# Performance work log

Measured on AMD Instinct MI355X. Metric: run time of the kernel, lower is better.

## Reference

```python
import jax, jax.numpy as jnp
import numpy as np

N = 8192
LATENT_DIM = 64


def setup_inputs() -> dict:
    key = jax.random.key(0)
    kx, ky = jax.random.split(key)
    x = jax.random.normal(kx, (N, LATENT_DIM), dtype=jnp.float32)
    y = jax.random.normal(ky, (N, LATENT_DIM), dtype=jnp.float32)
    return {"x": x, "y": y}


def _rbf_kernel(a, b):
    # Faithful to torch: exp(-mean((a_i - b_j)^2, axis=dim) / dim)
    #                  = exp(-||a_i - b_j||^2 / dim^2)
    # Computed via the expanded-sq-dist identity to avoid the [N, N, dim]
    # tiled intermediate the torch code materializes.
    dim = a.shape[1]
    sq_a = jnp.sum(a * a, axis=1)  # [Na]
    sq_b = jnp.sum(b * b, axis=1)  # [Nb]
    sq_dist = sq_a[:, None] + sq_b[None, :] - 2.0 * (a @ b.T)  # [Na, Nb]
    return jnp.exp(-sq_dist / (dim * dim))


def reference(x, y):
    # MMD with RBF kernel: mean k(x,x) + mean k(y,y) - 2 mean k(x,y)
    kxx = jnp.mean(_rbf_kernel(x, x))
    kyy = jnp.mean(_rbf_kernel(y, y))
    kxy = jnp.mean(_rbf_kernel(x, y))
    return kxx + kyy - 2.0 * kxy
```

## Files before the change

### kernel.cpp

```cpp
#include <hip/hip_runtime.h>
#include <cmath>

#define NPTS 8192
#define DIM 64
#define BT 128
#define KSTR 132

#define LEAF_F   0
#define LEAF_N   (3 * 8192 * 64)
#define ROWS_F   (LEAF_F + LEAF_N)
#define ROWS_N   (3 * 8192)
#define MEANS_F  (ROWS_F + ROWS_N)
#define NX_F     ((MEANS_F + 3 + 3) & ~3)
#define NY_F     (NX_F + 8192)
#define SPLIT_F  (NY_F + 8192)
#define SPLIT_ELEMS (NPTS * DIM)


typedef short bf16x8 __attribute__((ext_vector_type(8)));
typedef float f32x4  __attribute__((ext_vector_type(4)));
typedef float f32x2  __attribute__((ext_vector_type(2)));

__device__ __forceinline__ unsigned short f32_bf16_rne(float f) {
    unsigned u = __float_as_uint(f);
    return (unsigned short)((u + 0x7FFFu + ((u >> 16) & 1u)) >> 16);
}
__device__ __forceinline__ float bf16_f32(unsigned short h) {
    return __uint_as_float(((unsigned)h) << 16);
}

__global__ void prep_kernel(const float* __restrict__ x, const float* __restrict__ y,
                            unsigned short* __restrict__ Xh, unsigned short* __restrict__ Xl,
                            unsigned short* __restrict__ Yh, unsigned short* __restrict__ Yl,
                            float* __restrict__ nx, float* __restrict__ ny) {
    int r = blockIdx.x * 256 + threadIdx.x;
    int isY = r >= NPTS;
    int rr = isY ? r - NPTS : r;
    const float4* Rg = (const float4*)((isY ? y : x) + (size_t)rr * DIM);
    unsigned short* Hh = isY ? Yh : Xh;
    unsigned short* Hl = isY ? Yl : Xl;
    const int t16 = rr >> 4, mrow = rr & 15;
    float s = 0.f;
    #pragma unroll
    for (int k4 = 0; k4 < 16; ++k4) {
        float4 v = Rg[k4];
        ushort4 h, l;
        h.x = f32_bf16_rne(v.x); l.x = f32_bf16_rne(v.x - bf16_f32(h.x));
        h.y = f32_bf16_rne(v.y); l.y = f32_bf16_rne(v.y - bf16_f32(h.y));
        h.z = f32_bf16_rne(v.z); l.z = f32_bf16_rne(v.z - bf16_f32(h.z));
        h.w = f32_bf16_rne(v.w); l.w = f32_bf16_rne(v.w - bf16_f32(h.w));
        int off = t16 * 1024 + (k4 >> 3) * 512 + ((k4 >> 1) & 3) * 128 + mrow * 8 + (k4 & 1) * 4;
        *(ushort4*)(Hh + off) = h;
        *(ushort4*)(Hl + off) = l;
        s = fmaf(v.x, v.x, s); s = fmaf(v.y, v.y, s);
        s = fmaf(v.z, v.z, s); s = fmaf(v.w, v.w, s);
    }
    if (isY) ny[rr] = s; else nx[rr] = s;
}

__global__ __launch_bounds__(512, 4) void mmd_tile_kernel(
    const unsigned short* __restrict__ Xh, const unsigned short* __restrict__ Xl,
    const unsigned short* __restrict__ Yh, const unsigned short* __restrict__ Yl,
    const float* __restrict__ nx, const float* __restrict__ ny,
    float* __restrict__ leafs)
{
    const int gi = blockIdx.x;
    const int gj = blockIdx.y;
    int zz, bx, by;
    if (blockIdx.z == 1) {
        if (gi >= 64) return;
        zz = 2; bx = gi; by = gj;
    } else if (gi > gj) {
        zz = 0; by = gj; bx = gi - 1;
    } else {
        zz = 1; by = gi; bx = gj;
    }

    __shared__ __align__(16) float Ks[128 * KSTR];
    __shared__ float sqA[BT];
    __shared__ float sqB[BT];

    const int t = threadIdx.x;
    const size_t arow = (size_t)by * BT;
    const size_t brow = (size_t)bx * BT;
    const int cb = bx;

    const unsigned short* pAh = (zz == 1) ? Yh : Xh;
    const unsigned short* pAl = (zz == 1) ? Yl : Xl;
    const unsigned short* pBh = (zz == 0) ? Xh : Yh;
    const unsigned short* pBl = (zz == 0) ? Xl : Yl;

    if (t < 256) {
        const float* nA = (zz == 1) ? ny : nx;
        const float* nB = (zz == 0) ? nx : ny;
        if (t < BT) sqA[t] = nA[arow + t];
        else        sqB[t - BT] = nB[brow + t - BT];
    }
    __syncthreads();

    const int lane = t & 63;
    const int wv   = t >> 6;
    const int mrow = lane & 15;
    const int quad = lane >> 4;
    const int rblk = (wv & 3) << 5;
    const int cblk = (wv >> 2) << 6;

    const int aT = by * 8 + (wv & 3) * 2;
    const int bT = bx * 8 + (wv >> 2) * 4;
    const int lsub = quad * 128 + mrow * 8;

    bf16x8 fAh[2][2], fAl[2][2];
    #pragma unroll
    for (int rt = 0; rt < 2; ++rt)
        #pragma unroll
        for (int kc = 0; kc < 2; ++kc) {
            int off = (aT + rt) * 1024 + kc * 512 + lsub;
            fAh[rt][kc] = *(const bf16x8*)(pAh + off);
            fAl[rt][kc] = *(const bf16x8*)(pAl + off);
        }

    f32x4 acc[2][4];
    #pragma unroll
    for (int rt = 0; rt < 2; ++rt)
        #pragma unroll
        for (int ct = 0; ct < 4; ++ct)
            acc[rt][ct] = (f32x4){0.f, 0.f, 0.f, 0.f};

    #pragma unroll
    for (int ct = 0; ct < 4; ++ct) {
        int boff = (bT + ct) * 1024 + lsub;
        bf16x8 bh0 = *(const bf16x8*)(pBh + boff);
        bf16x8 bh1 = *(const bf16x8*)(pBh + boff + 512);
        bf16x8 bl0 = *(const bf16x8*)(pBl + boff);
        bf16x8 bl1 = *(const bf16x8*)(pBl + boff + 512);
        #pragma unroll
        for (int rt = 0; rt < 2; ++rt) {
            f32x4 c = acc[rt][ct];
            c = __builtin_amdgcn_mfma_f32_16x16x32_bf16(fAh[rt][0], bh0, c, 0, 0, 0);
            c = __builtin_amdgcn_mfma_f32_16x16x32_bf16(fAh[rt][0], bl0, c, 0, 0, 0);
            c = __builtin_amdgcn_mfma_f32_16x16x32_bf16(fAl[rt][0], bh0, c, 0, 0, 0);
            c = __builtin_amdgcn_mfma_f32_16x16x32_bf16(fAh[rt][1], bh1, c, 0, 0, 0);
            c = __builtin_amdgcn_mfma_f32_16x16x32_bf16(fAh[rt][1], bl1, c, 0, 0, 0);
            c = __builtin_amdgcn_mfma_f32_16x16x32_bf16(fAl[rt][1], bh1, c, 0, 0, 0);
            acc[rt][ct] = c;
        }
    }

    const float SCL = (float)(-1.4426950408889634 / 4096.0);
    #pragma unroll
    for (int rt = 0; rt < 2; ++rt)
        #pragma unroll
        for (int ct = 0; ct < 4; ++ct)
            #pragma unroll
            for (int i = 0; i < 4; ++i) {
                int row = rblk + rt * 16 + quad * 4 + i;
                int col = cblk + ct * 16 + mrow;
                float d  = acc[rt][ct][i];
                float s2 = sqA[row] + sqB[col];
                float sqd = s2 - 2.0f * d;
                Ks[row * KSTR + col] = exp2f(sqd * SCL);
            }
    __syncthreads();

    {
        int row = t >> 2;
        int tp  = t & 3;
        const float* base = &Ks[row * KSTR + 2 * tp];
        f32x2 v0 = *(const f32x2*)base;
        float se = v0.x, so = v0.y;
        #pragma unroll
        for (int q = 1; q < 16; ++q) {
            f32x2 v = *(const f32x2*)(base + 8 * q);
            se += v.x; so += v.y;
        }
        float s01 = se + so;
        float p;
        p = __shfl_xor(s01, 1); float s = s01 + p;
        p = __shfl_xor(s, 2);   s = s + p;
        if (tp == 0)
            leafs[((size_t)zz * 64 + cb) * 8192 + arow + row] = s;
    }

    if (zz < 2 && bx > by) {
        float mleaf[2];
        #pragma unroll
        for (int j = 0; j < 2; ++j) {
            int ch  = t + 512 * j;
            int c   = ch >> 3;
            int tt  = ch & 7;
            float s = Ks[tt * KSTR + c];
            #pragma unroll
            for (int q = 1; q < 16; ++q) s += Ks[(tt + 8 * q) * KSTR + c];
            float p;
            p = __shfl_xor(s, 1); s = s + p;
            p = __shfl_xor(s, 2); s = s + p;
            p = __shfl_xor(s, 4); s = s + p;
            mleaf[j] = s;
        }
        if ((t & 7) == 0) {
            int rb = t >> 3;
            #pragma unroll
            for (int j = 0; j < 2; ++j) {
                int row = rb + 64 * j;
                leafs[((size_t)zz * 64 + by) * 8192 + brow + row] = mleaf[j];
            }
        }
    }
}

__global__ void rowsum_kernel(const float* __restrict__ leafs, float* __restrict__ rowsums) {
    const int t = threadIdx.x;
    const int tid = blockIdx.x * 256 + t;
    const int z = tid >> 13;
    const int r = tid & 8191;
    const float* base = leafs + ((size_t)z * 64) * 8192 + r;
    float v[64];
    #pragma unroll
    for (int cbi = 0; cbi < 64; ++cbi) v[cbi] = base[(size_t)cbi * 8192];
    #pragma unroll
    for (int n = 32; n >= 1; n >>= 1)
        #pragma unroll
        for (int i = 0; i < 64; ++i)
            if (i < n) v[i] = v[2*i] + v[2*i+1];
    rowsums[tid] = v[0];
}

__global__ void colsum_kernel(const float* __restrict__ rowsums, float* __restrict__ means) {
    __shared__ float L[256];
    const int z = blockIdx.x;
    const int t = threadIdx.x;
    const float4* src = (const float4*)(rowsums + z * 8192);
    float w[32];
    #pragma unroll
    for (int i = 0; i < 8; ++i) {
        float4 q = src[t * 8 + i];
        w[4*i+0] = q.x; w[4*i+1] = q.y; w[4*i+2] = q.z; w[4*i+3] = q.w;
    }
    #pragma unroll
    for (int n = 16; n >= 1; n >>= 1)
        #pragma unroll
        for (int i = 0; i < 32; ++i)
            if (i < n) w[i] = w[2*i] + w[2*i+1];
    L[t] = w[0];
    __syncthreads();
    for (int n = 128; n >= 1; n >>= 1) {
        float u = 0.f;
        if (t < n) u = L[2*t] + L[2*t+1];
        __syncthreads();
        if (t < n) L[t] = u;
        __syncthreads();
    }
    if (t == 0) means[z] = L[0] * (1.0f / 67108864.0f);
}

__global__ void combine_kernel(const float* __restrict__ means, float* __restrict__ out) {
    float t1 = means[0] + means[1];
    out[0] = t1 - 2.0f * means[2];
}

extern "C" void kernel_launch(void* const* d_in, const int* in_sizes, int n_in,
                              void* d_out, int out_size, void* d_ws, size_t ws_size,
                              hipStream_t stream) {
    const float* x = (const float*)d_in[0];
    const float* y = (const float*)d_in[1];
    float* wsf     = (float*)d_ws;
    float* leafs   = wsf + LEAF_F;
    float* rowsums = wsf + ROWS_F;
    float* means   = wsf + MEANS_F;
    float* nx      = wsf + NX_F;
    float* ny      = wsf + NY_F;
    unsigned short* Xh = (unsigned short*)(wsf + SPLIT_F);
    unsigned short* Xl = Xh + SPLIT_ELEMS;
    unsigned short* Yh = Xl + SPLIT_ELEMS;
    unsigned short* Yl = Yh + SPLIT_ELEMS;

    prep_kernel<<<64, 256, 0, stream>>>(x, y, Xh, Xl, Yh, Yl, nx, ny);
    dim3 grid(65, 64, 2);
    mmd_tile_kernel<<<grid, 512, 0, stream>>>(Xh, Xl, Yh, Yl, nx, ny, leafs);
    rowsum_kernel<<<96, 256, 0, stream>>>(leafs, rowsums);
    colsum_kernel<<<3, 256, 0, stream>>>(rowsums, means);
    combine_kernel<<<1, 1, 0, stream>>>(means, (float*)d_out);
}
```

Measured before the change: 152.5 us.

## Reduce kernel tile in registers with shuffles instead of staging through LDS

Drops the 128x132 float shared-memory staging buffer for the exp'd kernel tile. Row and column partial sums are now computed in registers and combined with a transpose-style xor-shuffle reduction, then merged across waves through small shared arrays. This removes about 67KB of LDS per block and its read-back traffic, which could allow more resident blocks, at the cost of more shuffle instructions. The prep kernel launch also changes to 256 blocks of 64 threads.

```diff
diff --git a/kernel.cpp b/kernel.cpp
--- a/kernel.cpp
+++ b/kernel.cpp
@@ -4,7 +4,6 @@
 #define NPTS 8192
 #define DIM 64
 #define BT 128
-#define KSTR 132
 
 #define LEAF_F   0
 #define LEAF_N   (3 * 8192 * 64)
@@ -19,7 +18,6 @@
 
 typedef short bf16x8 __attribute__((ext_vector_type(8)));
 typedef float f32x4  __attribute__((ext_vector_type(4)));
-typedef float f32x2  __attribute__((ext_vector_type(2)));
 
 __device__ __forceinline__ unsigned short f32_bf16_rne(float f) {
     unsigned u = __float_as_uint(f);
@@ -33,7 +31,7 @@
                             unsigned short* __restrict__ Xh, unsigned short* __restrict__ Xl,
                             unsigned short* __restrict__ Yh, unsigned short* __restrict__ Yl,
                             float* __restrict__ nx, float* __restrict__ ny) {
-    int r = blockIdx.x * 256 + threadIdx.x;
+    int r = blockIdx.x * 64 + threadIdx.x;
     int isY = r >= NPTS;
     int rr = isY ? r - NPTS : r;
     const float4* Rg = (const float4*)((isY ? y : x) + (size_t)rr * DIM);
@@ -76,9 +74,10 @@
         zz = 1; by = gi; bx = gj;
     }
 
-    __shared__ __align__(16) float Ks[128 * KSTR];
     __shared__ float sqA[BT];
     __shared__ float sqB[BT];
+    __shared__ float rowpart[2][BT];
+    __shared__ float colpart[4][BT];
 
     const int t = threadIdx.x;
     const size_t arow = (size_t)by * BT;
@@ -147,6 +146,7 @@
     }
 
     const float SCL = (float)(-1.4426950408889634 / 4096.0);
+    float kk[2][4][4];
     #pragma unroll
     for (int rt = 0; rt < 2; ++rt)
         #pragma unroll
@@ -158,52 +158,76 @@
                 float d  = acc[rt][ct][i];
                 float s2 = sqA[row] + sqB[col];
                 float sqd = s2 - 2.0f * d;
-                Ks[row * KSTR + col] = exp2f(sqd * SCL);
+                kk[rt][ct][i] = exp2f(sqd * SCL);
             }
+
+    const bool domirror = (zz < 2) && (bx > by);
+
+    float rs[2][4];
+    #pragma unroll
+    for (int rt = 0; rt < 2; ++rt)
+        #pragma unroll
+        for (int i = 0; i < 4; ++i)
+            rs[rt][i] = (kk[rt][0][i] + kk[rt][1][i]) + (kk[rt][2][i] + kk[rt][3][i]);
+
+    float cs[4];
+    if (domirror) {
+        #pragma unroll
+        for (int ct = 0; ct < 4; ++ct)
+            cs[ct] = ((kk[0][ct][0] + kk[0][ct][1]) + (kk[0][ct][2] + kk[0][ct][3]))
+                   + ((kk[1][ct][0] + kk[1][ct][1]) + (kk[1][ct][2] + kk[1][ct][3]));
+    }
+
+    const int b0 = lane & 1;
+    const int b1 = (lane >> 1) & 1;
+    const int b2 = (lane >> 2) & 1;
+    const int b3 = (lane >> 3) & 1;
+
+    float a4[4];
+    #pragma unroll
+    for (int i = 0; i < 4; ++i) {
+        float snd = b3 ? rs[0][i] : rs[1][i];
+        float rcv = __shfl_xor(snd, 8);
+        a4[i] = (b3 ? rs[1][i] : rs[0][i]) + rcv;
+    }
+    float a2[2];
+    #pragma unroll
+    for (int j = 0; j < 2; ++j) {
+        float snd = b2 ? a4[j] : a4[2 + j];
+        float rcv = __shfl_xor(snd, 4);
+        a2[j] = (b2 ? a4[2 + j] : a4[j]) + rcv;
+    }
+    {
+        float snd = b1 ? a2[0] : a2[1];
+        float rcv = __shfl_xor(snd, 2);
+        float a1  = (b1 ? a2[1] : a2[0]) + rcv;
+        float r64 = a1 + __shfl_xor(a1, 1);
+        if (b0 == 0)
+            rowpart[wv >> 2][rblk + b3 * 16 + quad * 4 + b2 * 2 + b1] = r64;
+    }
+
+    if (domirror) {
+        const int b4 = (lane >> 4) & 1;
+        const int b5 = (lane >> 5) & 1;
+        float c2[2];
+        #pragma unroll
+        for (int j = 0; j < 2; ++j) {
+            float snd = b4 ? cs[j] : cs[2 + j];
+            float rcv = __shfl_xor(snd, 16);
+            c2[j] = (b4 ? cs[2 + j] : cs[j]) + rcv;
+        }
+        float snd = b5 ? c2[0] : c2[1];
+        float rcv = __shfl_xor(snd, 32);
+        float c1  = (b5 ? c2[1] : c2[0]) + rcv;
+        colpart[wv & 3][cblk + (b4 * 2 + b5) * 16 + mrow] = c1;
+    }
     __syncthreads();
 
-    {
-        int row = t >> 2;
-        int tp  = t & 3;
-        const float* base = &Ks[row * KSTR + 2 * tp];
-        f32x2 v0 = *(const f32x2*)base;
-        float se = v0.x, so = v0.y;
-        #pragma unroll
-        for (int q = 1; q < 16; ++q) {
-            f32x2 v = *(const f32x2*)(base + 8 * q);
-            se += v.x; so += v.y;
-        }
-        float s01 = se + so;
-        float p;
-        p = __shfl_xor(s01, 1); float s = s01 + p;
-        p = __shfl_xor(s, 2);   s = s + p;
-        if (tp == 0)
-            leafs[((size_t)zz * 64 + cb) * 8192 + arow + row] = s;
-    }
-
-    if (zz < 2 && bx > by) {
-        float mleaf[2];
-        #pragma unroll
-        for (int j = 0; j < 2; ++j) {
-            int ch  = t + 512 * j;
-            int c   = ch >> 3;
-            int tt  = ch & 7;
-            float s = Ks[tt * KSTR + c];
-            #pragma unroll
-            for (int q = 1; q < 16; ++q) s += Ks[(tt + 8 * q) * KSTR + c];
-            float p;
-            p = __shfl_xor(s, 1); s = s + p;
-            p = __shfl_xor(s, 2); s = s + p;
-            p = __shfl_xor(s, 4); s = s + p;
-            mleaf[j] = s;
-        }
-        if ((t & 7) == 0) {
-            int rb = t >> 3;
-            #pragma unroll
-            for (int j = 0; j < 2; ++j) {
-                int row = rb + 64 * j;
-                leafs[((size_t)zz * 64 + by) * 8192 + brow + row] = mleaf[j];
-            }
+    if (t < BT) {
+        leafs[((size_t)zz * 64 + cb) * 8192 + arow + t] = rowpart[0][t] + rowpart[1][t];
+        if (domirror) {
+            leafs[((size_t)zz * 64 + by) * 8192 + brow + t] =
+                (colpart[0][t] + colpart[1][t]) + (colpart[2][t] + colpart[3][t]);
         }
     }
 }
@@ -274,7 +298,7 @@
     unsigned short* Yh = Xl + SPLIT_ELEMS;
     unsigned short* Yl = Yh + SPLIT_ELEMS;
 
-    prep_kernel<<<64, 256, 0, stream>>>(x, y, Xh, Xl, Yh, Yl, nx, ny);
+    prep_kernel<<<256, 64, 0, stream>>>(x, y, Xh, Xl, Yh, Yl, nx, ny);
     dim3 grid(65, 64, 2);
     mmd_tile_kernel<<<grid, 512, 0, stream>>>(Xh, Xl, Yh, Yl, nx, ny, leafs);
     rowsum_kernel<<<96, 256, 0, stream>>>(leafs, rowsums);
```

Measured after the change: 146.5 us. 3.9% less time.
